# Kernel tuning notes

Hardware: AMD Instinct MI355X
Metric: run time of the kernel (lower is better)

## Reference

```python
import jax, jax.numpy as jnp
import numpy as np

N_NODES = 100000
N_EDGES = 600000
IN_FEATS = 128
HIDDEN = 128
OUT_DIM = 64
N_STEPS = 3


def _glorot(key, shape):
    fan_in, fan_out = shape[1], shape[0]
    lim = (6.0 / (fan_in + fan_out)) ** 0.5
    return jax.random.uniform(key, shape, jnp.float32, -lim, lim)


def setup_inputs() -> dict:
    key = jax.random.key(0)
    ks = jax.random.split(key, 12)
    x = jax.random.normal(ks[0], (N_NODES, IN_FEATS), jnp.float32)
    src = jax.random.randint(ks[1], (N_EDGES,), 0, N_NODES)
    dst = jax.random.randint(ks[2], (N_EDGES,), 0, N_NODES)
    return {
        "x": x,
        "src": src,
        "dst": dst,
        "W_in": _glorot(ks[3], (HIDDEN, IN_FEATS)),
        "b_in": jnp.zeros((HIDDEN,), jnp.float32),
        "W_e": _glorot(ks[4], (HIDDEN, HIDDEN)),
        "b_e": jnp.zeros((HIDDEN,), jnp.float32),
        "W_ih": _glorot(ks[5], (3 * HIDDEN, HIDDEN)),
        "b_ih": jnp.zeros((3 * HIDDEN,), jnp.float32),
        "W_hh": _glorot(ks[6], (3 * HIDDEN, HIDDEN)),
        "b_hh": jnp.zeros((3 * HIDDEN,), jnp.float32),
        "W_out": _glorot(ks[7], (OUT_DIM, HIDDEN)),
        "b_out": jnp.zeros((OUT_DIM,), jnp.float32),
    }


def _gru_cell(a, h, W_ih, b_ih, W_hh, b_hh):
    # torch.nn.GRUCell: gates ordered [reset, update, new]
    gi = a @ W_ih.T + b_ih          # [N, 3H]
    gh = h @ W_hh.T + b_hh          # [N, 3H]
    H = h.shape[-1]
    i_r, i_z, i_n = gi[:, :H], gi[:, H:2 * H], gi[:, 2 * H:]
    h_r, h_z, h_n = gh[:, :H], gh[:, H:2 * H], gh[:, 2 * H:]
    r = jax.nn.sigmoid(i_r + h_r)
    z = jax.nn.sigmoid(i_z + h_z)
    n = jnp.tanh(i_n + r * h_n)
    return (1.0 - z) * n + z * h


def reference(x, src, dst, W_in, b_in, W_e, b_e, W_ih, b_ih, W_hh, b_hh, W_out, b_out):
    # linear_in + relu (dropout is identity in eval mode)
    h = jax.nn.relu(x @ W_in.T + b_in)               # [N, H]
    for _ in range(N_STEPS):
        # single edge type: apply linear on all nodes, then gather per edge
        wh = h @ W_e.T + b_e                          # [N, H]
        msg = wh[src]                                 # [E, H] gather
        a = jax.ops.segment_sum(msg, dst, num_segments=N_NODES)  # scatter-add
        h = _gru_cell(a, h, W_ih, b_ih, W_hh, b_hh)
    return h @ W_out.T + b_out                        # [N, out_dim]
```

## Files before the change

### kernel.cpp

```cpp
#include <hip/hip_runtime.h>
#include <hip/hip_bf16.h>

#define N_NODES 100000
#define N_EDGES 600000
#define HID 128
#define OUTD 64

typedef unsigned short u16;
typedef unsigned int u32;
typedef __attribute__((ext_vector_type(8))) short bf16x8;
typedef __attribute__((ext_vector_type(4))) float f32x4;

__device__ __forceinline__ float bf2f(u16 u){
  union { u32 u; float f; } v; v.u = ((u32)u) << 16; return v.f;
}
__device__ __forceinline__ u16 f2bf(float f){
  union { float f; u32 u; } v; v.f = f;
  u32 r = v.u + 0x7fffu + ((v.u >> 16) & 1u);
  return (u16)(r >> 16);
}
__device__ __forceinline__ float sigf(float x){ return 1.f/(1.f + __expf(-x)); }
__device__ __forceinline__ float tanhfast(float x){ return 2.f/(1.f + __expf(-2.f*x)) - 1.f; }

__device__ __forceinline__ bf16x8 cvt8(const float* p){
  f32x4 a = *(const f32x4*)p;
  f32x4 b = *(const f32x4*)(p + 4);
  bf16x8 r;
  r[0]=(short)f2bf(a[0]); r[1]=(short)f2bf(a[1]); r[2]=(short)f2bf(a[2]); r[3]=(short)f2bf(a[3]);
  r[4]=(short)f2bf(b[0]); r[5]=(short)f2bf(b[1]); r[6]=(short)f2bf(b[2]); r[7]=(short)f2bf(b[3]);
  return r;
}

__global__ void k_hist(const int* __restrict__ dst, int* __restrict__ cnt){
  int e = blockIdx.x*256 + threadIdx.x;
  if (e < N_EDGES) atomicAdd(&cnt[dst[e]], 1);
}

__global__ void k_scan1(const int* __restrict__ cnt, int* __restrict__ part, int* __restrict__ bsum){
  __shared__ int s[256];
  int t = threadIdx.x, i = blockIdx.x*256 + t;
  int v = (i < N_NODES) ? cnt[i] : 0;
  s[t] = v; __syncthreads();
  for (int off = 1; off < 256; off <<= 1){
    int x = (t >= off) ? s[t-off] : 0;
    __syncthreads();
    s[t] += x;
    __syncthreads();
  }
  if (i < N_NODES) part[i] = s[t] - v;
  if (t == 255) bsum[blockIdx.x] = s[255];
}

__global__ void k_scan2(const int* __restrict__ bsum, int* __restrict__ boff, int nb){
  __shared__ int s[512];
  int t = threadIdx.x;
  int v = (t < nb) ? bsum[t] : 0;
  s[t] = v; __syncthreads();
  for (int off = 1; off < 512; off <<= 1){
    int x = (t >= off) ? s[t-off] : 0;
    __syncthreads();
    s[t] += x;
    __syncthreads();
  }
  if (t < nb) boff[t] = s[t] - v;
}

__global__ void k_scan3(const int* __restrict__ part, const int* __restrict__ boff, int* __restrict__ rp){
  int i = blockIdx.x*256 + threadIdx.x;
  if (i < N_NODES) rp[i] = part[i] + boff[i >> 8];
  if (i == 0) rp[N_NODES] = N_EDGES;
}

__global__ void k_fill(const int* __restrict__ src, const int* __restrict__ dst,
                       const int* __restrict__ rp, int* __restrict__ cur, int* __restrict__ eidx){
  int e = blockIdx.x*256 + threadIdx.x;
  if (e >= N_EDGES) return;
  int d = dst[e];
  int p = atomicAdd(&cur[d], 1);
  eidx[rp[d] + p] = src[e];
}

template<int NOUT, int RELU, int AFP32, int WBF, int WF32>
__global__ __launch_bounds__(256, 2) void k_gemm(
    const void* __restrict__ Av, const float* __restrict__ W, const float* __restrict__ bias,
    u16* __restrict__ Cb, float* __restrict__ Cf)
{
  constexpr int NT = NOUT/16;
  const int lane = threadIdx.x & 63;
  const int wib  = threadIdx.x >> 6;
  const int gw   = blockIdx.x * 4 + wib;
  const int nw   = gridDim.x * 4;
  const int ri   = lane & 15;
  const int kg   = lane >> 4;

  bf16x8 wf[NT][4];
  #pragma unroll
  for (int t = 0; t < NT; t++)
    #pragma unroll
    for (int kc = 0; kc < 4; kc++)
      wf[t][kc] = cvt8(W + (size_t)(t*16 + ri)*HID + kc*32 + kg*8);
  float bv[NT];
  #pragma unroll
  for (int t = 0; t < NT; t++) bv[t] = bias[t*16 + ri];

  for (int rc = gw; rc < N_NODES/16; rc += nw) {
    bf16x8 af[4];
    if (AFP32) {
      const float* ap = (const float*)Av + (size_t)(rc*16 + ri)*HID;
      #pragma unroll
      for (int kc = 0; kc < 4; kc++) af[kc] = cvt8(ap + kc*32 + kg*8);
    } else {
      const u16* ap = (const u16*)Av + (size_t)(rc*16 + ri)*HID;
      #pragma unroll
      for (int kc = 0; kc < 4; kc++) af[kc] = *(const bf16x8*)(ap + kc*32 + kg*8);
    }

    f32x4 acc[NT];
    #pragma unroll
    for (int t = 0; t < NT; t++) acc[t] = (f32x4){0.f,0.f,0.f,0.f};
    #pragma unroll
    for (int kc = 0; kc < 4; kc++)
      #pragma unroll
      for (int t = 0; t < NT; t++)
        acc[t] = __builtin_amdgcn_mfma_f32_16x16x32_bf16(af[kc], wf[t][kc], acc[t], 0, 0, 0);

    #pragma unroll
    for (int t = 0; t < NT; t++)
      #pragma unroll
      for (int j = 0; j < 4; j++){
        float v = acc[t][j] + bv[t];
        if (RELU) v = fmaxf(v, 0.f);
        int row = rc*16 + kg*4 + j;
        int col = t*16 + ri;
        if (WBF) Cb[(size_t)row*NOUT + col] = f2bf(v);
        if (WF32) Cf[(size_t)row*NOUT + col] = v;
      }
  }
}

__global__ void k_gather(const u16* __restrict__ wh, const int* __restrict__ rp,
                         const int* __restrict__ eidx, u16* __restrict__ a){
  int w   = (blockIdx.x * 256 + threadIdx.x) >> 6;
  int nwv = (gridDim.x * 256) >> 6;
  int lane = threadIdx.x & 63;
  for (int n = w; n < N_NODES; n += nwv){
    int s = rp[n], e = rp[n+1];
    float a0 = 0.f, a1 = 0.f;
    int i = s;
    for (; i + 1 < e; i += 2){
      int s0 = eidx[i], s1 = eidx[i+1];
      u32 v0 = *(const u32*)(wh + (size_t)s0*HID + lane*2);
      u32 v1 = *(const u32*)(wh + (size_t)s1*HID + lane*2);
      a0 += bf2f((u16)(v0 & 0xffffu)) + bf2f((u16)(v1 & 0xffffu));
      a1 += bf2f((u16)(v0 >> 16))     + bf2f((u16)(v1 >> 16));
    }
    if (i < e){
      int s0 = eidx[i];
      u32 v0 = *(const u32*)(wh + (size_t)s0*HID + lane*2);
      a0 += bf2f((u16)(v0 & 0xffffu));
      a1 += bf2f((u16)(v0 >> 16));
    }
    u32 o = ((u32)f2bf(a1) << 16) | (u32)f2bf(a0);
    *(u32*)(a + (size_t)n*HID + lane*2) = o;
  }
}

__global__ __launch_bounds__(512, 2) void k_gru(
    const u16* __restrict__ aB, const u16* __restrict__ hBin,
    const float* __restrict__ Wih, const float* __restrict__ Whh,
    const float* __restrict__ bih, const float* __restrict__ bhh,
    u16* __restrict__ hBout)
{
  const int lane = threadIdx.x & 63;
  const int ct   = threadIdx.x >> 6;
  const int ri   = lane & 15;
  const int kg   = lane >> 4;

  bf16x8 wf[6][4];
  #pragma unroll
  for (int g = 0; g < 3; g++)
    #pragma unroll
    for (int kc = 0; kc < 4; kc++){
      wf[g][kc]   = cvt8(Wih + (size_t)(g*HID + ct*16 + ri)*HID + kc*32 + kg*8);
      wf[3+g][kc] = cvt8(Whh + (size_t)(g*HID + ct*16 + ri)*HID + kc*32 + kg*8);
    }
  float bir = bih[ct*16+ri], biz = bih[HID+ct*16+ri], bin_ = bih[2*HID+ct*16+ri];
  float bhr = bhh[ct*16+ri], bhz = bhh[HID+ct*16+ri], bhn  = bhh[2*HID+ct*16+ri];

  for (int rc = blockIdx.x; rc < N_NODES/16; rc += gridDim.x) {
    const u16* ap = aB   + (size_t)(rc*16 + ri)*HID;
    const u16* hp = hBin + (size_t)(rc*16 + ri)*HID;
    bf16x8 af[4], hf[4];
    #pragma unroll
    for (int kc = 0; kc < 4; kc++){
      af[kc] = *(const bf16x8*)(ap + kc*32 + kg*8);
      hf[kc] = *(const bf16x8*)(hp + kc*32 + kg*8);
    }
    f32x4 acc[6];
    #pragma unroll
    for (int t = 0; t < 6; t++) acc[t] = (f32x4){0.f,0.f,0.f,0.f};
    #pragma unroll
    for (int kc = 0; kc < 4; kc++)
      #pragma unroll
      for (int g = 0; g < 3; g++){
        acc[g]   = __builtin_amdgcn_mfma_f32_16x16x32_bf16(af[kc], wf[g][kc],   acc[g],   0, 0, 0);
        acc[3+g] = __builtin_amdgcn_mfma_f32_16x16x32_bf16(hf[kc], wf[3+g][kc], acc[3+g], 0, 0, 0);
      }
    #pragma unroll
    for (int j = 0; j < 4; j++){
      float r  = sigf(acc[0][j] + bir + acc[3][j] + bhr);
      float z  = sigf(acc[1][j] + biz + acc[4][j] + bhz);
      float nn = tanhfast(acc[2][j] + bin_ + r*(acc[5][j] + bhn));
      int row = rc*16 + kg*4 + j;
      int col = ct*16 + ri;
      size_t idx = (size_t)row*HID + col;
      float ho = bf2f(hBin[idx]);
      float hn = (1.f - z)*nn + z*ho;
      hBout[idx] = f2bf(hn);
    }
  }
}

extern "C" void kernel_launch(void* const* d_in, const int* in_sizes, int n_in,
                              void* d_out, int out_size, void* d_ws, size_t ws_size,
                              hipStream_t stream)
{
  const float* x    = (const float*)d_in[0];
  const int*   src  = (const int*)d_in[1];
  const int*   dst  = (const int*)d_in[2];
  const float* Win  = (const float*)d_in[3];
  const float* bin  = (const float*)d_in[4];
  const float* We   = (const float*)d_in[5];
  const float* be   = (const float*)d_in[6];
  const float* Wih  = (const float*)d_in[7];
  const float* bih  = (const float*)d_in[8];
  const float* Whh  = (const float*)d_in[9];
  const float* bhh  = (const float*)d_in[10];
  const float* Wout = (const float*)d_in[11];
  const float* bout = (const float*)d_in[12];
  float* out = (float*)d_out;

  char* w = (char*)d_ws;
  auto alloc = [&](size_t bytes)->char*{ char* p = w; w += (bytes + 255) & ~(size_t)255; return p; };
  u16*   hB0 = (u16*)   alloc((size_t)N_NODES*HID*2);
  u16*   hB1 = (u16*)   alloc((size_t)N_NODES*HID*2);
  u16*   whB = (u16*)   alloc((size_t)N_NODES*HID*2);
  u16*   aB  = (u16*)   alloc((size_t)N_NODES*HID*2);
  int* cnt  = (int*)alloc((size_t)N_NODES*4);
  int* rp   = (int*)alloc((size_t)(N_NODES+1)*4);
  int* part = (int*)alloc((size_t)N_NODES*4);
  int* bsum = (int*)alloc(512*4);
  int* boff = (int*)alloc(512*4);
  int* cur  = (int*)alloc((size_t)N_NODES*4);
  int* eidx = (int*)alloc((size_t)N_EDGES*4);

  (void)hipMemsetAsync(cnt, 0, (size_t)N_NODES*4, stream);
  (void)hipMemsetAsync(cur, 0, (size_t)N_NODES*4, stream);

  const int eb = (N_EDGES + 255)/256;
  const int nb = (N_NODES + 255)/256;
  k_hist <<<eb, 256, 0, stream>>>(dst, cnt);
  k_scan1<<<nb, 256, 0, stream>>>(cnt, part, bsum);
  k_scan2<<<1, 512, 0, stream>>>(bsum, boff, nb);
  k_scan3<<<nb, 256, 0, stream>>>(part, boff, rp);
  k_fill <<<eb, 256, 0, stream>>>(src, dst, rp, cur, eidx);

  k_gemm<HID, 1, 1, 1, 0><<<1024, 256, 0, stream>>>((const void*)x, Win, bin, hB0, nullptr);

  u16* hcur = hB0; u16* hnxt = hB1;
  for (int s = 0; s < 3; s++){
    k_gemm<HID, 0, 0, 1, 0><<<1024, 256, 0, stream>>>((const void*)hcur, We, be, whB, nullptr);
    k_gather<<<2048, 256, 0, stream>>>(whB, rp, eidx, aB);
    k_gru<<<1024, 512, 0, stream>>>(aB, hcur, Wih, Whh, bih, bhh, hnxt);
    u16* t = hcur; hcur = hnxt; hnxt = t;
  }

  k_gemm<OUTD, 0, 0, 0, 1><<<1024, 256, 0, stream>>>((const void*)hcur, Wout, bout, nullptr, out);
}
```

Before: 706.0 us.

## Split GRU input and hidden GEMMs across separate waves via shared memory

The GRU kernel now runs 1024 threads per block. Half the waves compute the input-gate GEMM (a·W_ih) and the other half compute the hidden-gate GEMM (h·W_hh), so each wave holds only half of the weight fragments in registers. The input-gate results pass through double-buffered shared memory, with one __syncthreads per tile, to the hidden-side waves, which apply the gate math. This lowers register pressure so more waves can be resident, in exchange for LDS traffic and a block-wide barrier on every row tile.

```diff
diff --git a/kernel.cpp b/kernel.cpp
--- a/kernel.cpp
+++ b/kernel.cpp
@@ -165,59 +165,75 @@
   }
 }
 
-__global__ __launch_bounds__(512, 2) void k_gru(
+__global__ __launch_bounds__(1024, 4) void k_gru(
     const u16* __restrict__ aB, const u16* __restrict__ hBin,
     const float* __restrict__ Wih, const float* __restrict__ Whh,
     const float* __restrict__ bih, const float* __restrict__ bhh,
     u16* __restrict__ hBout)
 {
+  __shared__ float ls[2][8][12][64];
+
   const int lane = threadIdx.x & 63;
-  const int ct   = threadIdx.x >> 6;
+  const int wid  = threadIdx.x >> 6;
+  const int ct   = wid & 7;
+  const int isgh = wid >> 3;
   const int ri   = lane & 15;
   const int kg   = lane >> 4;
 
-  bf16x8 wf[6][4];
+  const float* Wm = isgh ? Whh : Wih;
+  bf16x8 wf[3][4];
   #pragma unroll
   for (int g = 0; g < 3; g++)
     #pragma unroll
-    for (int kc = 0; kc < 4; kc++){
-      wf[g][kc]   = cvt8(Wih + (size_t)(g*HID + ct*16 + ri)*HID + kc*32 + kg*8);
-      wf[3+g][kc] = cvt8(Whh + (size_t)(g*HID + ct*16 + ri)*HID + kc*32 + kg*8);
-    }
+    for (int kc = 0; kc < 4; kc++)
+      wf[g][kc] = cvt8(Wm + (size_t)(g*HID + ct*16 + ri)*HID + kc*32 + kg*8);
+
   float bir = bih[ct*16+ri], biz = bih[HID+ct*16+ri], bin_ = bih[2*HID+ct*16+ri];
   float bhr = bhh[ct*16+ri], bhz = bhh[HID+ct*16+ri], bhn  = bhh[2*HID+ct*16+ri];
 
+  int p = 0;
   for (int rc = blockIdx.x; rc < N_NODES/16; rc += gridDim.x) {
-    const u16* ap = aB   + (size_t)(rc*16 + ri)*HID;
-    const u16* hp = hBin + (size_t)(rc*16 + ri)*HID;
-    bf16x8 af[4], hf[4];
-    #pragma unroll
-    for (int kc = 0; kc < 4; kc++){
-      af[kc] = *(const bf16x8*)(ap + kc*32 + kg*8);
-      hf[kc] = *(const bf16x8*)(hp + kc*32 + kg*8);
-    }
-    f32x4 acc[6];
-    #pragma unroll
-    for (int t = 0; t < 6; t++) acc[t] = (f32x4){0.f,0.f,0.f,0.f};
-    #pragma unroll
-    for (int kc = 0; kc < 4; kc++)
-      #pragma unroll
-      for (int g = 0; g < 3; g++){
-        acc[g]   = __builtin_amdgcn_mfma_f32_16x16x32_bf16(af[kc], wf[g][kc],   acc[g],   0, 0, 0);
-        acc[3+g] = __builtin_amdgcn_mfma_f32_16x16x32_bf16(hf[kc], wf[3+g][kc], acc[3+g], 0, 0, 0);
+    const u16* srcp = (isgh ? hBin : aB) + (size_t)(rc*16 + ri)*HID;
+    bf16x8 xf[4];
+    #pragma unroll
+    for (int kc = 0; kc < 4; kc++)
+      xf[kc] = *(const bf16x8*)(srcp + kc*32 + kg*8);
+
+    f32x4 acc[3];
+    #pragma unroll
+    for (int g = 0; g < 3; g++) acc[g] = (f32x4){0.f,0.f,0.f,0.f};
+    #pragma unroll
+    for (int kc = 0; kc < 4; kc++)
+      #pragma unroll
+      for (int g = 0; g < 3; g++)
+        acc[g] = __builtin_amdgcn_mfma_f32_16x16x32_bf16(xf[kc], wf[g][kc], acc[g], 0, 0, 0);
+
+    if (!isgh){
+      #pragma unroll
+      for (int g = 0; g < 3; g++)
+        #pragma unroll
+        for (int j = 0; j < 4; j++)
+          ls[p][ct][g*4+j][lane] = acc[g][j];
+    }
+    __syncthreads();
+    if (isgh){
+      #pragma unroll
+      for (int j = 0; j < 4; j++){
+        float giR = ls[p][ct][0*4+j][lane];
+        float giZ = ls[p][ct][1*4+j][lane];
+        float giN = ls[p][ct][2*4+j][lane];
+        float r  = sigf(giR + bir + acc[0][j] + bhr);
+        float z  = sigf(giZ + biz + acc[1][j] + bhz);
+        float nn = tanhfast(giN + bin_ + r*(acc[2][j] + bhn));
+        int row = rc*16 + kg*4 + j;
+        int col = ct*16 + ri;
+        size_t idx = (size_t)row*HID + col;
+        float ho = bf2f(hBin[idx]);
+        float hn = (1.f - z)*nn + z*ho;
+        hBout[idx] = f2bf(hn);
       }
-    #pragma unroll
-    for (int j = 0; j < 4; j++){
-      float r  = sigf(acc[0][j] + bir + acc[3][j] + bhr);
-      float z  = sigf(acc[1][j] + biz + acc[4][j] + bhz);
-      float nn = tanhfast(acc[2][j] + bin_ + r*(acc[5][j] + bhn));
-      int row = rc*16 + kg*4 + j;
-      int col = ct*16 + ri;
-      size_t idx = (size_t)row*HID + col;
-      float ho = bf2f(hBin[idx]);
-      float hn = (1.f - z)*nn + z*ho;
-      hBout[idx] = f2bf(hn);
-    }
+    }
+    p ^= 1;
   }
 }
 
@@ -271,7 +287,7 @@
   for (int s = 0; s < 3; s++){
     k_gemm<HID, 0, 0, 1, 0><<<1024, 256, 0, stream>>>((const void*)hcur, We, be, whB, nullptr);
     k_gather<<<2048, 256, 0, stream>>>(whB, rp, eidx, aB);
-    k_gru<<<1024, 512, 0, stream>>>(aB, hcur, Wih, Whh, bih, bhh, hnxt);
+    k_gru<<<1024, 1024, 0, stream>>>(aB, hcur, Wih, Whh, bih, bhh, hnxt);
     u16* t = hcur; hcur = hnxt; hnxt = t;
   }
 
```

After: 723.9 us. 1.03x slower.
